# Performance work log

Measured on AMD Instinct MI355X. Metric: run time of the kernel, lower is better.

Reference implementation:

```python
import jax, jax.numpy as jnp
import numpy as np

B, S, D_IN, D_H, D_FF, E, D_OUT = 1024, 2048, 4, 16, 32, 8, 4

def setup_inputs() -> dict:
    key = jax.random.key(0)
    ks = jax.random.split(key, 8)
    return {
        "x":       jax.random.normal(ks[0], (B, S, D_IN), dtype=jnp.float32),
        "embed_w": jax.random.normal(ks[1], (D_H, D_IN), dtype=jnp.float32) / np.sqrt(D_IN),
        "embed_b": jnp.zeros((D_H,), dtype=jnp.float32),
        "gate_w":  jax.random.normal(ks[2], (D_H, E), dtype=jnp.float32) / np.sqrt(D_H),
        "wi":      jax.random.normal(ks[3], (E, D_H, D_FF), dtype=jnp.float32) / np.sqrt(D_H),
        "wo":      jax.random.normal(ks[4], (E, D_FF, D_H), dtype=jnp.float32) / np.sqrt(D_FF),
        "proj_w":  jax.random.normal(ks[5], (D_OUT, D_H), dtype=jnp.float32) / np.sqrt(D_H),
        "proj_b":  jnp.zeros((D_OUT,), dtype=jnp.float32),
    }

def reference(x, embed_w, embed_b, gate_w, wi, wo, proj_w, proj_b):
    # test_embed: Linear(4, 16)
    h = x @ embed_w.T + embed_b                      # [B, S, 16]
    t = h.reshape(-1, D_H)                           # [T, 16], T = B*S

    # SparseMLP top-1 router (softmax gate, no bias)
    probs = jax.nn.softmax(t @ gate_w, axis=-1)      # [T, E]
    top_idx = jnp.argmax(probs, axis=-1)             # [T] expert id
    top_p = jnp.max(probs, axis=-1)                  # [T] combine weight

    # Expert FFN (gelu MLP, no bias); small fixed loop over E=8 experts,
    # masked combine honors the top-1 dispatch structure.
    out = jnp.zeros_like(t)
    for e in range(E):
        y_e = jax.nn.gelu(t @ wi[e]) @ wo[e]         # [T, 16]
        out = out + jnp.where((top_idx == e)[:, None], y_e, 0.0)
    out = out * top_p[:, None]                       # combine with gate prob
    out = out.reshape(B, S, D_H)

    # proj: Linear(16, 4)
    return out @ proj_w.T + proj_b                   # [B, S, 4]
```

## Files before the change

kernel.cpp:

```cpp
#include <hip/hip_runtime.h>

constexpr int TOK      = 1024 * 2048;
constexpr int NTHREADS = 2048 * 256;
constexpr int ITERS    = TOK / NTHREADS;

typedef float f32x4 __attribute__((ext_vector_type(4)));
typedef float f32x2 __attribute__((ext_vector_type(2)));

constexpr int WS_FLOATS = 2348;

__global__ void setup_fused(
    const float* __restrict__ ew,
    const float* __restrict__ eb,
    const float* __restrict__ gw,
    const float* __restrict__ wi,
    const float* __restrict__ wo,
    const float* __restrict__ pw,
    const float* __restrict__ pb,
    float* __restrict__ ws)
{
    int idx = blockIdx.x * blockDim.x + threadIdx.x;
    if (idx >= WS_FLOATS) return;
    float v = 0.0f;
    if (idx < 32) {
        int k = idx >> 3, j = idx & 7;
        for (int i = 0; i < 16; ++i) v += ew[i * 4 + k] * gw[i * 8 + j];
    } else if (idx < 40) {
        int j = idx - 32;
        for (int i = 0; i < 16; ++i) v += eb[i] * gw[i * 8 + j];
    } else if (idx < 1064) {
        int r = idx - 40; int e = r >> 7, k = (r >> 5) & 3, f = r & 31;
        for (int i = 0; i < 16; ++i) v += ew[i * 4 + k] * wi[(e * 16 + i) * 32 + f];
    } else if (idx < 1320) {
        int r = idx - 1064; int e = r >> 5, f = r & 31;
        for (int i = 0; i < 16; ++i) v += eb[i] * wi[(e * 16 + i) * 32 + f];
    } else if (idx < 2344) {
        int r = idx - 1320; int e = r >> 7, f = (r >> 2) & 31, o = r & 3;
        for (int i = 0; i < 16; ++i) v += wo[(e * 32 + f) * 16 + i] * pw[o * 16 + i];
    } else {
        v = pb[idx - 2344];
    }
    ws[idx] = v;
}

constexpr int WF_STRIDE = 132;
constexpr int UB_STRIDE = 36;
constexpr int PF_STRIDE = 132;

__device__ __forceinline__ f32x4 splat4(float s) { return (f32x4){s, s, s, s}; }

__global__ __launch_bounds__(256) void moe_main(
    const float* __restrict__ x,
    const float* __restrict__ ws,
    float* __restrict__ out)
{
    __shared__ __align__(16) float sG[48];
    __shared__ __align__(16) float sWf[8 * WF_STRIDE];
    __shared__ __align__(16) float sUb[8 * UB_STRIDE];
    __shared__ __align__(16) float sPf[8 * PF_STRIDE];

    const int tid = threadIdx.x;

    if (tid < 44) sG[tid] = ws[tid < 40 ? tid : (2344 + tid - 40)];
    {
        int i = tid;
        #pragma unroll
        for (int rep = 0; rep < 4; ++rep, i += 256) {
            int e = i >> 7, r = i & 127;
            sWf[e * WF_STRIDE + r] = ws[40 + i];
            sPf[e * PF_STRIDE + r] = ws[1320 + i];
        }
    }
    {
        int e = tid >> 5, r = tid & 31;
        sUb[e * UB_STRIDE + r] = ws[1064 + tid];
    }
    __syncthreads();

    const f32x4* __restrict__ x4 = (const f32x4*)x;
    f32x4* __restrict__ o4       = (f32x4*)out;

    f32x4 Gr[8];
    #pragma unroll
    for (int q = 0; q < 8; ++q) Gr[q] = ((const f32x4*)sG)[q];
    f32x4 w_gb0 = ((const f32x4*)sG)[8];
    f32x4 w_gb1 = ((const f32x4*)sG)[9];
    f32x4 w_pb  = ((const f32x4*)sG)[10];

    constexpr float LOG2E  = 1.4426950408889634f;
    constexpr float GELU_K = 2.3025850929940457f;
    constexpr float GELU_B = 0.044715f;
    const f32x4 one4 = splat4(1.0f);

    int t = blockIdx.x * blockDim.x + tid;
    for (int it = 0; it < ITERS; ++it, t += NTHREADS) {
        f32x4 xv = x4[t];

        f32x4 ga = w_gb0, gb2 = w_gb1;
        #pragma unroll
        for (int k = 0; k < 4; ++k) {
            f32x4 xs = splat4(xv[k]);
            ga  = __builtin_elementwise_fma(xs, Gr[2 * k],     ga);
            gb2 = __builtin_elementwise_fma(xs, Gr[2 * k + 1], gb2);
        }
        float g[8] = {ga[0], ga[1], ga[2], ga[3], gb2[0], gb2[1], gb2[2], gb2[3]};

        float gmax = g[0]; int e = 0;
        #pragma unroll
        for (int j = 1; j < 8; ++j) {
            if (g[j] > gmax) { gmax = g[j]; e = j; }
        }
        float ssum = 0.0f;
        #pragma unroll
        for (int j = 0; j < 8; ++j)
            ssum += __builtin_amdgcn_exp2f((g[j] - gmax) * LOG2E);
        float top_p = __builtin_amdgcn_rcpf(ssum);

        const f32x4* wfe = (const f32x4*)(sWf + e * WF_STRIDE);
        const f32x4* ube = (const f32x4*)(sUb + e * UB_STRIDE);
        const f32x4* pfe = (const f32x4*)(sPf + e * PF_STRIDE);

        f32x4 U[8];
        #pragma unroll
        for (int q = 0; q < 8; ++q) U[q] = ube[q];
        #pragma unroll
        for (int k = 0; k < 4; ++k) {
            f32x4 xs = splat4(xv[k]);
            #pragma unroll
            for (int q = 0; q < 8; ++q)
                U[q] = __builtin_elementwise_fma(xs, wfe[k * 8 + q], U[q]);
        }

        #pragma unroll
        for (int q = 0; q < 8; ++q) {
            f32x4 v  = U[q];
            f32x4 m  = __builtin_elementwise_fma(v * splat4(GELU_B), v, one4);
            f32x4 a  = (v * splat4(GELU_K)) * m;
            f32x4 tt;
            #pragma unroll
            for (int c = 0; c < 4; ++c) tt[c] = __builtin_amdgcn_exp2f(a[c]);
            tt = tt + one4;
            f32x4 r;
            #pragma unroll
            for (int c = 0; c < 4; ++c) r[c] = __builtin_amdgcn_rcpf(tt[c]);
            U[q] = __builtin_elementwise_fma(-v, r, v);
        }

        f32x4 acc = splat4(0.0f);
        #pragma unroll
        for (int q = 0; q < 8; ++q) {
            #pragma unroll
            for (int c = 0; c < 4; ++c)
                acc = __builtin_elementwise_fma(splat4(U[q][c]), pfe[q * 4 + c], acc);
        }
        o4[t] = __builtin_elementwise_fma(splat4(top_p), acc, w_pb);
    }
}

extern "C" void kernel_launch(void* const* d_in, const int* in_sizes, int n_in,
                              void* d_out, int out_size, void* d_ws, size_t ws_size,
                              hipStream_t stream) {
    const float* x  = (const float*)d_in[0];
    const float* ew = (const float*)d_in[1];
    const float* eb = (const float*)d_in[2];
    const float* gw = (const float*)d_in[3];
    const float* wi = (const float*)d_in[4];
    const float* wo = (const float*)d_in[5];
    const float* pw = (const float*)d_in[6];
    const float* pb = (const float*)d_in[7];
    float* ws  = (float*)d_ws;
    float* out = (float*)d_out;

    setup_fused<<<(WS_FLOATS + 255) / 256, 256, 0, stream>>>(ew, eb, gw, wi, wo, pw, pb, ws);
    moe_main<<<NTHREADS / 256, 256, 0, stream>>>(x, ws, out);
}
```

Baseline: 45.83 us.

## Sort tokens by expert within each block and use wave-uniform weight loads

Each block now handles 1024 tokens. It first routes them all and counts them per expert using ballots and shared atomics, then scatters token ids into expert-sorted order. The expert FFN then runs on sorted tokens, and each wave loops over the distinct experts it holds, reading weights with a wave-uniform index straight from global memory instead of from per-lane indexed LDS. This targets divergent LDS weight reads, but it adds a routing pass, extra barriers, a second read of x, and scattered, uncoalesced output writes.

After: 115.6 us. 152% more time.

```diff
diff --git a/kernel.cpp b/kernel.cpp
--- a/kernel.cpp
+++ b/kernel.cpp
@@ -1,11 +1,12 @@
 #include <hip/hip_runtime.h>
 
-constexpr int TOK      = 1024 * 2048;
-constexpr int NTHREADS = 2048 * 256;
-constexpr int ITERS    = TOK / NTHREADS;
+constexpr int TOK     = 1024 * 2048;
+constexpr int TPB     = 256;
+constexpr int TOK_PB  = 1024;
+constexpr int ITERS   = TOK_PB / TPB;
+constexpr int NBLK    = TOK / TOK_PB;
 
 typedef float f32x4 __attribute__((ext_vector_type(4)));
-typedef float f32x2 __attribute__((ext_vector_type(2)));
 
 constexpr int WS_FLOATS = 2348;
 
@@ -43,10 +44,6 @@
     ws[idx] = v;
 }
 
-constexpr int WF_STRIDE = 132;
-constexpr int UB_STRIDE = 36;
-constexpr int PF_STRIDE = 132;
-
 __device__ __forceinline__ f32x4 splat4(float s) { return (f32x4){s, s, s, s}; }
 
 __global__ __launch_bounds__(256) void moe_main(
@@ -54,47 +51,41 @@
     const float* __restrict__ ws,
     float* __restrict__ out)
 {
-    __shared__ __align__(16) float sG[48];
-    __shared__ __align__(16) float sWf[8 * WF_STRIDE];
-    __shared__ __align__(16) float sUb[8 * UB_STRIDE];
-    __shared__ __align__(16) float sPf[8 * PF_STRIDE];
-
-    const int tid = threadIdx.x;
-
-    if (tid < 44) sG[tid] = ws[tid < 40 ? tid : (2344 + tid - 40)];
-    {
-        int i = tid;
-        #pragma unroll
-        for (int rep = 0; rep < 4; ++rep, i += 256) {
-            int e = i >> 7, r = i & 127;
-            sWf[e * WF_STRIDE + r] = ws[40 + i];
-            sPf[e * PF_STRIDE + r] = ws[1320 + i];
-        }
-    }
-    {
-        int e = tid >> 5, r = tid & 31;
-        sUb[e * UB_STRIDE + r] = ws[1064 + tid];
-    }
-    __syncthreads();
-
+    __shared__ float        s_p[TOK_PB];
+    __shared__ unsigned int s_sid[TOK_PB];
+    __shared__ int          s_cnt[8];
+    __shared__ int          s_base[8];
+
+    const int tid  = threadIdx.x;
+    const int lane = tid & 63;
+    const unsigned long long lt_mask = (lane == 63) ? 0x7fffffffffffffffull
+                                                    : ((1ull << lane) - 1ull);
+
+    if (tid < 8) s_cnt[tid] = 0;
+    __syncthreads();
+
+    const int gbase = blockIdx.x * TOK_PB;
     const f32x4* __restrict__ x4 = (const f32x4*)x;
     f32x4* __restrict__ o4       = (f32x4*)out;
 
     f32x4 Gr[8];
     #pragma unroll
-    for (int q = 0; q < 8; ++q) Gr[q] = ((const f32x4*)sG)[q];
-    f32x4 w_gb0 = ((const f32x4*)sG)[8];
-    f32x4 w_gb1 = ((const f32x4*)sG)[9];
-    f32x4 w_pb  = ((const f32x4*)sG)[10];
+    for (int q = 0; q < 8; ++q) Gr[q] = ((const f32x4*)ws)[q];
+    const f32x4 w_gb0 = ((const f32x4*)ws)[8];
+    const f32x4 w_gb1 = ((const f32x4*)ws)[9];
+    const f32x4 w_pb  = ((const f32x4*)(ws + 2344))[0];
 
     constexpr float LOG2E  = 1.4426950408889634f;
     constexpr float GELU_K = 2.3025850929940457f;
     constexpr float GELU_B = 0.044715f;
     const f32x4 one4 = splat4(1.0f);
 
-    int t = blockIdx.x * blockDim.x + tid;
-    for (int it = 0; it < ITERS; ++it, t += NTHREADS) {
-        f32x4 xv = x4[t];
+    int e_arr[ITERS], pos_arr[ITERS];
+
+    #pragma unroll
+    for (int it = 0; it < ITERS; ++it) {
+        const int t_loc = it * TPB + tid;
+        f32x4 xv = x4[gbase + t_loc];
 
         f32x4 ga = w_gb0, gb2 = w_gb1;
         #pragma unroll
@@ -107,53 +98,105 @@
 
         float gmax = g[0]; int e = 0;
         #pragma unroll
-        for (int j = 1; j < 8; ++j) {
+        for (int j = 1; j < 8; ++j)
             if (g[j] > gmax) { gmax = g[j]; e = j; }
-        }
         float ssum = 0.0f;
         #pragma unroll
         for (int j = 0; j < 8; ++j)
             ssum += __builtin_amdgcn_exp2f((g[j] - gmax) * LOG2E);
-        float top_p = __builtin_amdgcn_rcpf(ssum);
-
-        const f32x4* wfe = (const f32x4*)(sWf + e * WF_STRIDE);
-        const f32x4* ube = (const f32x4*)(sUb + e * UB_STRIDE);
-        const f32x4* pfe = (const f32x4*)(sPf + e * PF_STRIDE);
-
-        f32x4 U[8];
-        #pragma unroll
-        for (int q = 0; q < 8; ++q) U[q] = ube[q];
-        #pragma unroll
-        for (int k = 0; k < 4; ++k) {
-            f32x4 xs = splat4(xv[k]);
-            #pragma unroll
-            for (int q = 0; q < 8; ++q)
-                U[q] = __builtin_elementwise_fma(xs, wfe[k * 8 + q], U[q]);
+        s_p[t_loc] = __builtin_amdgcn_rcpf(ssum);
+
+        int pos_w = 0, my_cnt = 0;
+        #pragma unroll
+        for (int j = 0; j < 8; ++j) {
+            unsigned long long bj = __ballot(e == j);
+            int pc_lt = __popcll(bj & lt_mask);
+            int pc    = __popcll(bj);
+            if (e == j)    pos_w  = pc_lt;
+            if (lane == j) my_cnt = pc;
         }
-
-        #pragma unroll
-        for (int q = 0; q < 8; ++q) {
-            f32x4 v  = U[q];
-            f32x4 m  = __builtin_elementwise_fma(v * splat4(GELU_B), v, one4);
-            f32x4 a  = (v * splat4(GELU_K)) * m;
-            f32x4 tt;
-            #pragma unroll
-            for (int c = 0; c < 4; ++c) tt[c] = __builtin_amdgcn_exp2f(a[c]);
-            tt = tt + one4;
-            f32x4 r;
-            #pragma unroll
-            for (int c = 0; c < 4; ++c) r[c] = __builtin_amdgcn_rcpf(tt[c]);
-            U[q] = __builtin_elementwise_fma(-v, r, v);
+        int base_w = 0;
+        if (lane < 8) base_w = atomicAdd(&s_cnt[lane], my_cnt);
+        int base = __shfl(base_w, e, 64);
+        e_arr[it]   = e;
+        pos_arr[it] = base + pos_w;
+    }
+    __syncthreads();
+
+    if (tid == 0) {
+        int run = 0;
+        #pragma unroll
+        for (int j = 0; j < 8; ++j) { s_base[j] = run; run += s_cnt[j]; }
+    }
+    __syncthreads();
+
+    #pragma unroll
+    for (int it = 0; it < ITERS; ++it) {
+        const int t_loc = it * TPB + tid;
+        const int slot  = s_base[e_arr[it]] + pos_arr[it];
+        s_sid[slot] = (unsigned)t_loc | ((unsigned)e_arr[it] << 16);
+    }
+    __syncthreads();
+
+    #pragma unroll 1
+    for (int it = 0; it < ITERS; ++it) {
+        const unsigned v  = s_sid[it * TPB + tid];
+        const int sid  = (int)(v & 0xffffu);
+        const int eTok = (int)(v >> 16);
+
+        f32x4 xv = x4[gbase + sid];
+        float tp = s_p[sid];
+
+        bool done = false;
+        while (true) {
+            unsigned long long act = __ballot(!done);
+            if (act == 0) break;
+            int src = (int)__builtin_ctzll(act);
+            int e0  = __shfl(eTok, src, 64);
+            e0 = __builtin_amdgcn_readfirstlane(e0);
+
+            if (!done && eTok == e0) {
+                const f32x4* __restrict__ wf4 = (const f32x4*)(ws + 40   + e0 * 128);
+                const f32x4* __restrict__ ub4 = (const f32x4*)(ws + 1064 + e0 * 32);
+                const f32x4* __restrict__ pf4 = (const f32x4*)(ws + 1320 + e0 * 128);
+
+                f32x4 U[8];
+                #pragma unroll
+                for (int q = 0; q < 8; ++q) U[q] = ub4[q];
+                #pragma unroll
+                for (int k = 0; k < 4; ++k) {
+                    f32x4 xs = splat4(xv[k]);
+                    #pragma unroll
+                    for (int q = 0; q < 8; ++q)
+                        U[q] = __builtin_elementwise_fma(xs, wf4[k * 8 + q], U[q]);
+                }
+
+                #pragma unroll
+                for (int q = 0; q < 8; ++q) {
+                    f32x4 vv = U[q];
+                    f32x4 m  = __builtin_elementwise_fma(vv * splat4(GELU_B), vv, one4);
+                    f32x4 a  = (vv * splat4(GELU_K)) * m;
+                    f32x4 tt;
+                    #pragma unroll
+                    for (int c = 0; c < 4; ++c) tt[c] = __builtin_amdgcn_exp2f(a[c]);
+                    tt = tt + one4;
+                    f32x4 r;
+                    #pragma unroll
+                    for (int c = 0; c < 4; ++c) r[c] = __builtin_amdgcn_rcpf(tt[c]);
+                    U[q] = __builtin_elementwise_fma(-vv, r, vv);
+                }
+
+                f32x4 acc = splat4(0.0f);
+                #pragma unroll
+                for (int q = 0; q < 8; ++q) {
+                    #pragma unroll
+                    for (int c = 0; c < 4; ++c)
+                        acc = __builtin_elementwise_fma(splat4(U[q][c]), pf4[q * 4 + c], acc);
+                }
+                o4[gbase + sid] = __builtin_elementwise_fma(splat4(tp), acc, w_pb);
+                done = true;
+            }
         }
-
-        f32x4 acc = splat4(0.0f);
-        #pragma unroll
-        for (int q = 0; q < 8; ++q) {
-            #pragma unroll
-            for (int c = 0; c < 4; ++c)
-                acc = __builtin_elementwise_fma(splat4(U[q][c]), pfe[q * 4 + c], acc);
-        }
-        o4[t] = __builtin_elementwise_fma(splat4(top_p), acc, w_pb);
     }
 }
 
@@ -172,5 +215,5 @@
     float* out = (float*)d_out;
 
     setup_fused<<<(WS_FLOATS + 255) / 256, 256, 0, stream>>>(ew, eb, gw, wi, wo, pw, pb, ws);
-    moe_main<<<NTHREADS / 256, 256, 0, stream>>>(x, ws, out);
+    moe_main<<<NBLK, TPB, 0, stream>>>(x, ws, out);
 }
```

## Pack expert weights to fp16 and use packed dot2 for expert matmuls

Applied to the files above, without the earlier changes.

Expert input and output weight matrices (folded with the embed and proj layers) are now stored as packed fp16 pairs. The per-token matmuls use v_dot2 (fdot2) on fp16-converted activations instead of fp32 FMAs, which halves the LDS traffic and the matmul instruction count. Gate and bias values are now read straight from global memory instead of LDS. Rounding the activations and gelu outputs to fp16 with round-toward-zero adds error, which could exceed tolerance.

After: 46.75 us. +2.0%, slower.

```diff
diff --git a/kernel.cpp b/kernel.cpp
--- a/kernel.cpp
+++ b/kernel.cpp
@@ -1,13 +1,22 @@
 #include <hip/hip_runtime.h>
 
-constexpr int TOK      = 1024 * 2048;
-constexpr int NTHREADS = 2048 * 256;
-constexpr int ITERS    = TOK / NTHREADS;
-
-typedef float f32x4 __attribute__((ext_vector_type(4)));
-typedef float f32x2 __attribute__((ext_vector_type(2)));
-
-constexpr int WS_FLOATS = 2348;
+constexpr int TOK   = 1024 * 2048;
+constexpr int TPB   = 256;
+constexpr int NBLK  = 2048;
+constexpr int ITERS = TOK / (NBLK * TPB);
+
+typedef float  f32x4 __attribute__((ext_vector_type(4)));
+typedef __fp16 h2    __attribute__((ext_vector_type(2)));
+
+constexpr int OFF_GF = 0, OFF_GB = 32, OFF_PB = 40;
+constexpr int OFF_WF = 44, OFF_UB = 556, OFF_PF = 684, WS_W = 1196;
+constexpr int WF_S = 68, UB_S = 20, PF_S = 68;
+
+__device__ __forceinline__ unsigned pk16(float a, float b) {
+    unsigned ua = (unsigned)__builtin_bit_cast(unsigned short, (__fp16)a);
+    unsigned ub = (unsigned)__builtin_bit_cast(unsigned short, (__fp16)b);
+    return ua | (ub << 16);
+}
 
 __global__ void setup_fused(
     const float* __restrict__ ew,
@@ -17,83 +26,96 @@
     const float* __restrict__ wo,
     const float* __restrict__ pw,
     const float* __restrict__ pb,
-    float* __restrict__ ws)
+    unsigned* __restrict__ wsu)
 {
     int idx = blockIdx.x * blockDim.x + threadIdx.x;
-    if (idx >= WS_FLOATS) return;
-    float v = 0.0f;
-    if (idx < 32) {
+    if (idx >= WS_W) return;
+    float* wsf = (float*)wsu;
+    if (idx < OFF_GB) {
         int k = idx >> 3, j = idx & 7;
+        float v = 0.f;
         for (int i = 0; i < 16; ++i) v += ew[i * 4 + k] * gw[i * 8 + j];
-    } else if (idx < 40) {
-        int j = idx - 32;
+        wsf[idx] = v;
+    } else if (idx < OFF_PB) {
+        int j = idx - OFF_GB;
+        float v = 0.f;
         for (int i = 0; i < 16; ++i) v += eb[i] * gw[i * 8 + j];
-    } else if (idx < 1064) {
-        int r = idx - 40; int e = r >> 7, k = (r >> 5) & 3, f = r & 31;
-        for (int i = 0; i < 16; ++i) v += ew[i * 4 + k] * wi[(e * 16 + i) * 32 + f];
-    } else if (idx < 1320) {
-        int r = idx - 1064; int e = r >> 5, f = r & 31;
-        for (int i = 0; i < 16; ++i) v += eb[i] * wi[(e * 16 + i) * 32 + f];
-    } else if (idx < 2344) {
-        int r = idx - 1320; int e = r >> 7, f = (r >> 2) & 31, o = r & 3;
-        for (int i = 0; i < 16; ++i) v += wo[(e * 32 + f) * 16 + i] * pw[o * 16 + i];
+        wsf[idx] = v;
+    } else if (idx < OFF_WF) {
+        wsf[idx] = pb[idx - OFF_PB];
+    } else if (idx < OFF_UB) {
+        int r = idx - OFF_WF; int e = r >> 6, t = r & 63, f = t >> 1, p = t & 1;
+        float v0 = 0.f, v1 = 0.f;
+        for (int i = 0; i < 16; ++i) {
+            float w = wi[(e * 16 + i) * 32 + f];
+            v0 += ew[i * 4 + 2 * p]     * w;
+            v1 += ew[i * 4 + 2 * p + 1] * w;
+        }
+        wsu[idx] = pk16(v0, v1);
+    } else if (idx < OFF_PF) {
+        int r = idx - OFF_UB; int e = r >> 4, j = r & 15;
+        float v0 = 0.f, v1 = 0.f;
+        for (int i = 0; i < 16; ++i) {
+            v0 += eb[i] * wi[(e * 16 + i) * 32 + 2 * j];
+            v1 += eb[i] * wi[(e * 16 + i) * 32 + 2 * j + 1];
+        }
+        wsu[idx] = pk16(v0, v1);
     } else {
-        v = pb[idx - 2344];
-    }
-    ws[idx] = v;
-}
-
-constexpr int WF_STRIDE = 132;
-constexpr int UB_STRIDE = 36;
-constexpr int PF_STRIDE = 132;
+        int r = idx - OFF_PF; int e = r >> 6, t = r & 63, j = t >> 2, o = t & 3;
+        float v0 = 0.f, v1 = 0.f;
+        for (int i = 0; i < 16; ++i) {
+            float p = pw[o * 16 + i];
+            v0 += wo[(e * 32 + 2 * j)     * 16 + i] * p;
+            v1 += wo[(e * 32 + 2 * j + 1) * 16 + i] * p;
+        }
+        wsu[idx] = pk16(v0, v1);
+    }
+}
 
 __device__ __forceinline__ f32x4 splat4(float s) { return (f32x4){s, s, s, s}; }
+__device__ __forceinline__ h2 bch2(unsigned u) { return __builtin_bit_cast(h2, u); }
 
 __global__ __launch_bounds__(256) void moe_main(
     const float* __restrict__ x,
-    const float* __restrict__ ws,
+    const unsigned* __restrict__ wsu,
     float* __restrict__ out)
 {
-    __shared__ __align__(16) float sG[48];
-    __shared__ __align__(16) float sWf[8 * WF_STRIDE];
-    __shared__ __align__(16) float sUb[8 * UB_STRIDE];
-    __shared__ __align__(16) float sPf[8 * PF_STRIDE];
-
+    __shared__ __align__(16) unsigned sWf[8 * WF_S];
+    __shared__ __align__(16) unsigned sUb[8 * UB_S];
+    __shared__ __align__(16) unsigned sPf[8 * PF_S];
+
+    const float* wsf = (const float*)wsu;
     const int tid = threadIdx.x;
 
-    if (tid < 44) sG[tid] = ws[tid < 40 ? tid : (2344 + tid - 40)];
-    {
-        int i = tid;
-        #pragma unroll
-        for (int rep = 0; rep < 4; ++rep, i += 256) {
-            int e = i >> 7, r = i & 127;
-            sWf[e * WF_STRIDE + r] = ws[40 + i];
-            sPf[e * PF_STRIDE + r] = ws[1320 + i];
-        }
-    }
-    {
-        int e = tid >> 5, r = tid & 31;
-        sUb[e * UB_STRIDE + r] = ws[1064 + tid];
-    }
-    __syncthreads();
+    for (int i = tid; i < 512; i += TPB) {
+        int e = i >> 6, r = i & 63;
+        sWf[e * WF_S + r] = wsu[OFF_WF + i];
+        sPf[e * PF_S + r] = wsu[OFF_PF + i];
+    }
+    if (tid < 128) {
+        int e = tid >> 4, r = tid & 15;
+        sUb[e * UB_S + r] = wsu[OFF_UB + tid];
+    }
 
     const f32x4* __restrict__ x4 = (const f32x4*)x;
     f32x4* __restrict__ o4       = (f32x4*)out;
 
     f32x4 Gr[8];
     #pragma unroll
-    for (int q = 0; q < 8; ++q) Gr[q] = ((const f32x4*)sG)[q];
-    f32x4 w_gb0 = ((const f32x4*)sG)[8];
-    f32x4 w_gb1 = ((const f32x4*)sG)[9];
-    f32x4 w_pb  = ((const f32x4*)sG)[10];
+    for (int q = 0; q < 8; ++q) Gr[q] = ((const f32x4*)wsf)[q];
+    const f32x4 w_gb0 = ((const f32x4*)wsf)[8];
+    const f32x4 w_gb1 = ((const f32x4*)wsf)[9];
+    const f32x4 w_pb  = *(const f32x4*)(wsf + OFF_PB);
 
     constexpr float LOG2E  = 1.4426950408889634f;
     constexpr float GELU_K = 2.3025850929940457f;
     constexpr float GELU_B = 0.044715f;
     const f32x4 one4 = splat4(1.0f);
 
-    int t = blockIdx.x * blockDim.x + tid;
-    for (int it = 0; it < ITERS; ++it, t += NTHREADS) {
+    __syncthreads();
+
+    int t = blockIdx.x * TPB + tid;
+    for (int it = 0; it < ITERS; ++it, t += NBLK * TPB) {
         f32x4 xv = x4[t];
 
         f32x4 ga = w_gb0, gb2 = w_gb1;
@@ -107,53 +129,79 @@
 
         float gmax = g[0]; int e = 0;
         #pragma unroll
-        for (int j = 1; j < 8; ++j) {
+        for (int j = 1; j < 8; ++j)
             if (g[j] > gmax) { gmax = g[j]; e = j; }
-        }
         float ssum = 0.0f;
         #pragma unroll
         for (int j = 0; j < 8; ++j)
             ssum += __builtin_amdgcn_exp2f((g[j] - gmax) * LOG2E);
-        float top_p = __builtin_amdgcn_rcpf(ssum);
-
-        const f32x4* wfe = (const f32x4*)(sWf + e * WF_STRIDE);
-        const f32x4* ube = (const f32x4*)(sUb + e * UB_STRIDE);
-        const f32x4* pfe = (const f32x4*)(sPf + e * PF_STRIDE);
-
-        f32x4 U[8];
-        #pragma unroll
-        for (int q = 0; q < 8; ++q) U[q] = ube[q];
-        #pragma unroll
-        for (int k = 0; k < 4; ++k) {
-            f32x4 xs = splat4(xv[k]);
-            #pragma unroll
-            for (int q = 0; q < 8; ++q)
-                U[q] = __builtin_elementwise_fma(xs, wfe[k * 8 + q], U[q]);
-        }
-
-        #pragma unroll
-        for (int q = 0; q < 8; ++q) {
-            f32x4 v  = U[q];
-            f32x4 m  = __builtin_elementwise_fma(v * splat4(GELU_B), v, one4);
-            f32x4 a  = (v * splat4(GELU_K)) * m;
+        float tp = __builtin_amdgcn_rcpf(ssum);
+
+        h2 x01 = __builtin_amdgcn_cvt_pkrtz(xv[0], xv[1]);
+        h2 x23 = __builtin_amdgcn_cvt_pkrtz(xv[2], xv[3]);
+
+        const uint4* __restrict__ wf4 = (const uint4*)(sWf + e * WF_S);
+        const uint4* __restrict__ ub4 = (const uint4*)(sUb + e * UB_S);
+        const uint4* __restrict__ pf4 = (const uint4*)(sPf + e * PF_S);
+
+        uint4 ubv0 = ub4[0], ubv1 = ub4[1], ubv2 = ub4[2], ubv3 = ub4[3];
+        unsigned ubw[16] = {ubv0.x, ubv0.y, ubv0.z, ubv0.w,
+                            ubv1.x, ubv1.y, ubv1.z, ubv1.w,
+                            ubv2.x, ubv2.y, ubv2.z, ubv2.w,
+                            ubv3.x, ubv3.y, ubv3.z, ubv3.w};
+
+        f32x4 Ug[8];
+        #pragma unroll
+        for (int j = 0; j < 8; ++j) {
+            uint4 wa = wf4[2 * j];
+            uint4 wb = wf4[2 * j + 1];
+            h2 hb0 = bch2(ubw[2 * j]);
+            h2 hb1 = bch2(ubw[2 * j + 1]);
+            f32x4 U;
+            U[0] = __builtin_amdgcn_fdot2(x01, bch2(wa.x),
+                     __builtin_amdgcn_fdot2(x23, bch2(wa.y), (float)hb0.x, false), false);
+            U[1] = __builtin_amdgcn_fdot2(x01, bch2(wa.z),
+                     __builtin_amdgcn_fdot2(x23, bch2(wa.w), (float)hb0.y, false), false);
+            U[2] = __builtin_amdgcn_fdot2(x01, bch2(wb.x),
+                     __builtin_amdgcn_fdot2(x23, bch2(wb.y), (float)hb1.x, false), false);
+            U[3] = __builtin_amdgcn_fdot2(x01, bch2(wb.z),
+                     __builtin_amdgcn_fdot2(x23, bch2(wb.w), (float)hb1.y, false), false);
+            Ug[j] = U;
+        }
+
+        #pragma unroll
+        for (int j = 0; j < 8; ++j) {
+            f32x4 vv = Ug[j];
+            f32x4 m  = __builtin_elementwise_fma(vv * splat4(GELU_B), vv, one4);
+            f32x4 a  = (vv * splat4(GELU_K)) * m;
             f32x4 tt;
             #pragma unroll
-            for (int c = 0; c < 4; ++c) tt[c] = __builtin_amdgcn_exp2f(a[c]);
+            for (int q = 0; q < 4; ++q) tt[q] = __builtin_amdgcn_exp2f(a[q]);
             tt = tt + one4;
             f32x4 r;
             #pragma unroll
-            for (int c = 0; c < 4; ++c) r[c] = __builtin_amdgcn_rcpf(tt[c]);
-            U[q] = __builtin_elementwise_fma(-v, r, v);
+            for (int q = 0; q < 4; ++q) r[q] = __builtin_amdgcn_rcpf(tt[q]);
+            Ug[j] = __builtin_elementwise_fma(-vv, r, vv);
         }
 
         f32x4 acc = splat4(0.0f);
         #pragma unroll
-        for (int q = 0; q < 8; ++q) {
-            #pragma unroll
-            for (int c = 0; c < 4; ++c)
-                acc = __builtin_elementwise_fma(splat4(U[q][c]), pfe[q * 4 + c], acc);
-        }
-        o4[t] = __builtin_elementwise_fma(splat4(top_p), acc, w_pb);
+        for (int j = 0; j < 8; ++j) {
+            h2 a01 = __builtin_amdgcn_cvt_pkrtz(Ug[j][0], Ug[j][1]);
+            h2 a23 = __builtin_amdgcn_cvt_pkrtz(Ug[j][2], Ug[j][3]);
+            uint4 p0 = pf4[2 * j];
+            uint4 p1 = pf4[2 * j + 1];
+            acc[0] = __builtin_amdgcn_fdot2(a01, bch2(p0.x), acc[0], false);
+            acc[1] = __builtin_amdgcn_fdot2(a01, bch2(p0.y), acc[1], false);
+            acc[2] = __builtin_amdgcn_fdot2(a01, bch2(p0.z), acc[2], false);
+            acc[3] = __builtin_amdgcn_fdot2(a01, bch2(p0.w), acc[3], false);
+            acc[0] = __builtin_amdgcn_fdot2(a23, bch2(p1.x), acc[0], false);
+            acc[1] = __builtin_amdgcn_fdot2(a23, bch2(p1.y), acc[1], false);
+            acc[2] = __builtin_amdgcn_fdot2(a23, bch2(p1.z), acc[2], false);
+            acc[3] = __builtin_amdgcn_fdot2(a23, bch2(p1.w), acc[3], false);
+        }
+
+        o4[t] = __builtin_elementwise_fma(splat4(tp), acc, w_pb);
     }
 }
 
@@ -168,9 +216,9 @@
     const float* wo = (const float*)d_in[5];
     const float* pw = (const float*)d_in[6];
     const float* pb = (const float*)d_in[7];
-    float* ws  = (float*)d_ws;
-    float* out = (float*)d_out;
-
-    setup_fused<<<(WS_FLOATS + 255) / 256, 256, 0, stream>>>(ew, eb, gw, wi, wo, pw, pb, ws);
-    moe_main<<<NTHREADS / 256, 256, 0, stream>>>(x, ws, out);
-}
+    unsigned* wsu = (unsigned*)d_ws;
+    float* out    = (float*)d_out;
+
+    setup_fused<<<(WS_W + 255) / 256, 256, 0, stream>>>(ew, eb, gw, wi, wo, pw, pb, wsu);
+    moe_main<<<NBLK, TPB, 0, stream>>>(x, wsu, out);
+}
```
